# Optimization experiments

Hardware: AMD Instinct MI355X
Metric: run time of the kernel (lower is better)

## Reference

```python
import jax, jax.numpy as jnp
import numpy as np

B, L = 4, 2048
D_MODEL, D_INNER, D_STATE, DT_RANK, K = 512, 1024, 16, 64, 4


def setup_inputs() -> dict:
    key = jax.random.key(0)
    ks = jax.random.split(key, 21)
    def n(k, shape, s=0.02):
        return (jax.random.normal(k, shape) * s).astype(jnp.float32)
    inp = {"x": jax.random.normal(ks[0], (B, L, D_MODEL), jnp.float32)}
    for i, sfx in enumerate(("f", "b")):
        o = 1 + i * 8
        inp[f"W_in_{sfx}"] = n(ks[o], (2 * D_INNER, D_MODEL))
        inp[f"conv_w_{sfx}"] = n(ks[o + 1], (D_INNER, 1, K), 0.1)
        inp[f"conv_b_{sfx}"] = jnp.zeros((D_INNER,), jnp.float32)
        inp[f"A_log_{sfx}"] = (jax.random.normal(ks[o + 2], (D_STATE, D_INNER)) * 0.1).astype(jnp.float32)
        inp[f"D_{sfx}"] = jnp.ones((D_INNER,), jnp.float32)
        inp[f"Wx_{sfx}"] = n(ks[o + 3], (DT_RANK + 2 * D_STATE, D_INNER))
        inp[f"Wdt_{sfx}"] = n(ks[o + 4], (D_INNER, DT_RANK), DT_RANK ** -0.5)
        dt = jnp.exp(jax.random.uniform(ks[o + 5], (D_INNER,)) * (np.log(0.1) - np.log(0.001)) + np.log(0.001))
        inp[f"bdt_{sfx}"] = (dt + jnp.log(-jnp.expm1(-dt))).astype(jnp.float32)
        inp[f"Wout_{sfx}"] = n(ks[o + 6], (D_MODEL, D_INNER))
    return inp


def _mamba_block(x, W_in, conv_w, conv_b, A_log, Dp, Wx, Wdt, bdt, Wout):
    # x: [B, L, d_model]
    xz = jnp.einsum('bld,ed->ble', x, W_in)              # [B, L, 2*d_inner]
    xb, zb = xz[..., :D_INNER], xz[..., D_INNER:]
    # causal depthwise conv over time
    xc = jnp.transpose(xb, (0, 2, 1))                     # [B, M, L]
    xc = jax.lax.conv_general_dilated(
        xc, conv_w, window_strides=(1,), padding=[(K - 1, 0)],
        feature_group_count=D_INNER,
        dimension_numbers=('NCH', 'OIH', 'NCH')) + conv_b[None, :, None]
    xb = jax.nn.silu(jnp.transpose(xc, (0, 2, 1)))        # [B, L, M]
    # input-dependent SSM parameters
    proj = jnp.einsum('blm,pm->blp', xb, Wx)              # [B, L, dt_rank+2D]
    dt_in = proj[..., :DT_RANK]
    Bs = proj[..., DT_RANK:DT_RANK + D_STATE]             # [B, L, D]
    Cs = proj[..., DT_RANK + D_STATE:]                    # [B, L, D]
    dt = jax.nn.softplus(jnp.einsum('blr,mr->blm', dt_in, Wdt) + bdt)  # [B, L, M]
    A_T = -jnp.exp(A_log).T                               # [M, D]

    def step(h, inp):
        dt_t, x_t, B_t, C_t = inp                         # [B,M],[B,M],[B,D],[B,D]
        dA = jnp.exp(dt_t[:, :, None] * A_T[None])        # [B, M, D]
        h = dA * h + (dt_t * x_t)[:, :, None] * B_t[:, None, :]
        y_t = jnp.einsum('bmd,bd->bm', h, C_t)
        return h, y_t

    xs = (jnp.moveaxis(dt, 1, 0), jnp.moveaxis(xb, 1, 0),
          jnp.moveaxis(Bs, 1, 0), jnp.moveaxis(Cs, 1, 0))
    h0 = jnp.zeros((x.shape[0], D_INNER, D_STATE), x.dtype)
    _, ys = jax.lax.scan(step, h0, xs)                    # [L, B, M]
    y = jnp.moveaxis(ys, 0, 1) + Dp * xb                  # [B, L, M]
    y = y * jax.nn.silu(zb)                               # SiLU gate
    return jnp.einsum('blm,dm->bld', y, Wout)             # [B, L, d_model]


def reference(x,
              W_in_f, conv_w_f, conv_b_f, A_log_f, D_f, Wx_f, Wdt_f, bdt_f, Wout_f,
              W_in_b, conv_w_b, conv_b_b, A_log_b, D_b, Wx_b, Wdt_b, bdt_b, Wout_b):
    out_f = _mamba_block(x, W_in_f, conv_w_f, conv_b_f, A_log_f, D_f, Wx_f, Wdt_f, bdt_f, Wout_f)
    out_b = jnp.flip(_mamba_block(jnp.flip(x, 1), W_in_b, conv_w_b, conv_b_b, A_log_b, D_b, Wx_b, Wdt_b, bdt_b, Wout_b), 1)
    return out_f + out_b
```

## Files before the change

### kernel.cpp

```cpp
#include <hip/hip_runtime.h>
#include <hip/hip_bf16.h>
#include <cstdint>
#include <cstdio>

typedef float f32x4 __attribute__((ext_vector_type(4)));
typedef short s16x8 __attribute__((ext_vector_type(8)));
typedef unsigned int u32x2 __attribute__((ext_vector_type(2)));

__device__ __forceinline__ float us2f(unsigned short u){
  union { unsigned int i; float f; } v; v.i = ((unsigned int)u) << 16; return v.f;
}
__device__ __forceinline__ unsigned short f2us(float f){
  union { float f; unsigned int i; } v; v.f = f;
  unsigned int r = v.i + 0x7fffu + ((v.i >> 16) & 1u);
  return (unsigned short)(r >> 16);
}
__device__ __forceinline__ void gload_lds16(const void* g, void* l){
  __builtin_amdgcn_global_load_lds(
      (const __attribute__((address_space(1))) unsigned int*)g,
      (__attribute__((address_space(3))) unsigned int*)l, 16, 0, 0);
}

#define PK0 0.999962f

__global__ __launch_bounds__(256)
void prep_k(const float* __restrict__ x,
            const float* __restrict__ W_in_f, const float* __restrict__ W_in_b,
            const float* __restrict__ Wx_f,   const float* __restrict__ Wx_b,
            const float* __restrict__ Wdt_f,  const float* __restrict__ Wdt_b,
            const float* __restrict__ Wout_f, const float* __restrict__ Wout_b,
            const float* __restrict__ Alog_f, const float* __restrict__ Alog_b,
            const float* __restrict__ bdt_f,  const float* __restrict__ bdt_b,
            unsigned short* __restrict__ W1cat, unsigned short* __restrict__ Wxpad,
            unsigned short* __restrict__ Wdtb,  unsigned short* __restrict__ Woutcat,
            float* __restrict__ A2, float* __restrict__ bdtcat,
            unsigned short* __restrict__ xbf, float* __restrict__ Cf)
{
  long i = (long)blockIdx.x * 256 + threadIdx.x;
  if (i < 4194304) {
    xbf[i] = f2us(x[i]); return;
  }
  i -= 4194304;
  if (i < 2097152) {
    int n = (int)(i >> 9), k = (int)(i & 511);
    float v = (n < 2048) ? W_in_f[(long)n*512 + k] : W_in_b[(long)(n-2048)*512 + k];
    W1cat[i] = f2us(v); return;
  }
  i -= 2097152;
  if (i < 262144) {
    int dir = (int)(i >> 17); long r = i & 131071; int n = (int)(r >> 10), k = (int)(r & 1023);
    const float* Wx = dir ? Wx_b : Wx_f;
    Wxpad[(long)dir*131072 + r] = f2us(n < 96 ? Wx[(long)n*1024 + k] : 0.f); return;
  }
  i -= 262144;
  if (i < 131072) {
    int dir = (int)(i >> 16); long r = i & 65535;
    Wdtb[i] = f2us((dir ? Wdt_b : Wdt_f)[r]); return;
  }
  i -= 131072;
  if (i < 1048576) {
    int n = (int)(i >> 11), k = (int)(i & 2047);
    float v = (k < 1024) ? Wout_f[(long)n*1024 + k] : Wout_b[(long)n*1024 + (k-1024)];
    Woutcat[i] = f2us(v); return;
  }
  i -= 1048576;
  if (i < 32768) {
    int dir = (int)(i >> 14); long r = i & 16383; int m = (int)(r >> 4), d = (int)(r & 15);
    const float* Al = dir ? Alog_b : Alog_f;
    A2[i] = -__expf(Al[(long)d*1024 + m]) * 1.4426950408889634f; return;
  }
  i -= 32768;
  if (i < 2048) {
    int dir = (int)(i >> 10), m = (int)(i & 1023);
    bdtcat[i] = (dir ? bdt_b : bdt_f)[m]; return;
  }
  i -= 2048;
  if (i < 98304) {
    int dir = (int)(i / 49152); long r = i % 49152;
    int m = (int)(r / 48), j = (int)(r % 48);
    int k = j >> 4, d = j & 15;
    const float* Al = dir ? Alog_b : Alog_f;
    const float w = -__expf(Al[(long)d*1024 + m]);
    float c;
    if (k == 0)      c = 0.999150f * w;
    else if (k == 1) c = 0.492809f * w * w;
    else             c = 0.139212f * w * w * w;
    Cf[(long)dir*49152 + (long)m*48 + (k << 4) + d] = c;
    return;
  }
}

template<int OUT_MODE, int DBUF>
__global__ __launch_bounds__(256)
void gemm_bt(const unsigned short* __restrict__ Ap, const unsigned short* __restrict__ Bp,
             void* __restrict__ Cp, const float* __restrict__ biasp,
             float* __restrict__ bcf,
             int K, int lda, int ldb, int ldc,
             long az, long bz, long cz, int biasz)
{
  const int z   = blockIdx.z;
  const int tid = threadIdx.x;
  const int bm  = blockIdx.x, bn = blockIdx.y;

  __shared__ __align__(16) unsigned short Ash[1+DBUF][128][64];
  __shared__ __align__(16) unsigned short Bsh[1+DBUF][128][64];

  const int wave = tid >> 6, lane = tid & 63;
  const int wr = (wave >> 1) << 6, wc = (wave & 1) << 6;
  const int fr = lane & 15, fs = lane >> 4;

  const int rr  = tid >> 3;
  const int csp = tid & 7;
  const int csg = ((csp ^ (rr & 7)) << 3);

  const unsigned short* Ag = Ap + (long)z * az;
  const unsigned short* Bg = Bp + (long)z * bz;

  const long abase = (long)(bm*128 + rr)*lda + csg;
  const long bbase = (long)(bn*128 + rr)*ldb + csg;

  f32x4 acc[4][4];
  #pragma unroll
  for (int i=0;i<4;i++)
    #pragma unroll
    for (int j=0;j<4;j++) acc[i][j] = (f32x4){0.f,0.f,0.f,0.f};

  const int NK = K >> 6;

  auto stage = [&](int buf, int ks){
    const long k0 = (long)ks << 6;
    #pragma unroll
    for (int r=0;r<4;r++){
      gload_lds16(Ag + abase + (long)(r*32)*lda + k0, &Ash[buf][rr + r*32][csp << 3]);
      gload_lds16(Bg + bbase + (long)(r*32)*ldb + k0, &Bsh[buf][rr + r*32][csp << 3]);
    }
  };
  auto compute = [&](int buf){
    #pragma unroll
    for (int sub=0; sub<2; ++sub){
      s16x8 af[4], bfv[4];
      #pragma unroll
      for (int i=0;i<4;i++){
        const int ar = wr + i*16 + fr;
        af[i]  = *(const s16x8*)&Ash[buf][ar][(((sub<<2)+fs) ^ (fr&7)) << 3];
        const int br = wc + i*16 + fr;
        bfv[i] = *(const s16x8*)&Bsh[buf][br][(((sub<<2)+fs) ^ (fr&7)) << 3];
      }
      #pragma unroll
      for (int i=0;i<4;i++)
        #pragma unroll
        for (int j=0;j<4;j++)
          acc[i][j] = __builtin_amdgcn_mfma_f32_16x16x32_bf16(bfv[j], af[i], acc[i][j], 0, 0, 0);
    }
  };

  if (DBUF){
    stage(0, 0);
    int cur = 0;
    for (int ks = 0; ks < NK; ++ks){
      __syncthreads();
      if (ks + 1 < NK) stage(cur ^ 1, ks + 1);
      compute(cur);
      cur ^= 1;
    }
  } else {
    for (int ks = 0; ks < NK; ++ks){
      __syncthreads();
      stage(0, ks);
      __syncthreads();
      compute(0);
    }
  }

  #pragma unroll
  for (int i=0;i<4;i++){
    const int row = bm*128 + wr + i*16 + fr;
    #pragma unroll
    for (int j=0;j<4;j++){
      const int c0 = bn*128 + wc + j*16 + (fs << 2);
      f32x4 v = acc[i][j];
      const long cbase = (long)z*cz + (long)row*ldc + c0;
      if (OUT_MODE == 2){
        *(f32x4*)((float*)Cp + cbase) = v;
      } else if (OUT_MODE == 1){
        const f32x4 b4 = *(const f32x4*)(biasp + z*biasz + c0);
        u32x2 o;
        unsigned short s[4];
        #pragma unroll
        for (int e=0;e<4;e++){
          float t = v[e] + b4[e];
          t = fmaxf(t, 0.f) + log1pf(__expf(-fabsf(t)));
          s[e] = f2us(t);
        }
        o[0] = (unsigned int)s[0] | ((unsigned int)s[1] << 16);
        o[1] = (unsigned int)s[2] | ((unsigned int)s[3] << 16);
        *(u32x2*)((unsigned short*)Cp + cbase) = o;
      } else {
        if (OUT_MODE == 4 && ((c0 >> 10) & 1)){
          #pragma unroll
          for (int e=0;e<4;e++) v[e] = v[e] / (1.f + __expf(-v[e]));
        }
        u32x2 o;
        o[0] = (unsigned int)f2us(v[0]) | ((unsigned int)f2us(v[1]) << 16);
        o[1] = (unsigned int)f2us(v[2]) | ((unsigned int)f2us(v[3]) << 16);
        *(u32x2*)((unsigned short*)Cp + cbase) = o;
        if (OUT_MODE == 3 && c0 >= 64 && c0 < 96){
          *(f32x4*)(bcf + ((long)z*8192 + row)*32 + (c0 - 64)) = v;
        }
      }
    }
  }
}

__global__ __launch_bounds__(256)
void conv_silu_k(const unsigned short* __restrict__ xz,
                 const float* __restrict__ wf, const float* __restrict__ cbf,
                 const float* __restrict__ wb, const float* __restrict__ cbb,
                 unsigned short* __restrict__ xbc)
{
  const int tid = threadIdx.x;
  const long tok = blockIdx.x;
  const int l   = (int)(tok & 2047);
  const int dir = tid >> 7;
  const int mg  = (tid & 127) << 3;
  const float* w  = dir ? wb  : wf;
  const float* cb = dir ? cbb : cbf;
  const long rowb = tok << 12;
  const int  xcol = (dir << 11) + mg;

  f32x4 wv[8];
  #pragma unroll
  for (int e=0;e<8;e++) wv[e] = *(const f32x4*)(w + (mg + e)*4);
  const f32x4 cb0 = *(const f32x4*)(cb + mg);
  const f32x4 cb1 = *(const f32x4*)(cb + mg + 4);

  float acc[8];
  #pragma unroll
  for (int e=0;e<4;e++){ acc[e]=cb0[e]; acc[4+e]=cb1[e]; }

  #pragma unroll
  for (int k=0;k<4;k++){
    const int off = dir ? (3 - k) : (k - 3);
    const int pos = l + off;
    if (pos >= 0 && pos < 2048){
      const s16x8 xv = *(const s16x8*)(xz + rowb + ((long)off << 12) + xcol);
      #pragma unroll
      for (int e=0;e<8;e++)
        acc[e] = __builtin_fmaf(wv[e][k], us2f((unsigned short)xv[e]), acc[e]);
    }
  }
  s16x8 out;
  #pragma unroll
  for (int e=0;e<8;e++){
    const float s = acc[e] / (1.f + __expf(-acc[e]));
    out[e] = (short)f2us(s);
  }
  *(s16x8*)(xbc + tok*2048 + (dir << 10) + mg) = out;
}

#define SCHUNK 32
#define NCHUNK 64

__global__ __launch_bounds__(256)
void scan1_k(const unsigned short* __restrict__ dtb, const unsigned short* __restrict__ xbc,
             const float* __restrict__ BCf, const float* __restrict__ Cf,
             unsigned short* __restrict__ hloc, float* __restrict__ Ssum)
{
  const int tidx = threadIdx.x;
  const int cb = blockIdx.x, c = blockIdx.y, bz = blockIdx.z;
  const int b = bz >> 1, dir = bz & 1;
  const int m = cb*256 + tidx;

  float C1[16], C2[16], C3[16];
  { const f32x4* p = (const f32x4*)(Cf + ((long)dir*1024 + m)*48);
    #pragma unroll
    for (int q=0;q<4;q++){
      f32x4 v1=p[q], v2=p[q+4], v3=p[q+8];
      #pragma unroll
      for (int e=0;e<4;e++){ C1[q*4+e]=v1[e]; C2[q*4+e]=v2[e]; C3[q*4+e]=v3[e]; } } }

  const int  l0 = dir ? (2047 - c*SCHUNK) : (c*SCHUNK);
  const int  ls = dir ? -1 : 1;
  const long tok0 = (long)b*2048 + l0;

  __shared__ float Bs[SCHUNK][16];
  if (tidx < 128){
    const int r = tidx >> 2, c4 = (tidx & 3) << 2;
    *(f32x4*)&Bs[r][c4] =
        *(const f32x4*)(BCf + ((long)dir*8192 + tok0 + (long)ls*r)*32 + c4);
  }
  __syncthreads();

  const unsigned short* dtp = dtb + ((long)dir << 23) + tok0*1024 + m;
  const unsigned short* xvp = xbc + tok0*2048 + (dir << 10) + m;
  const long dstp = (long)ls*1024, xstp = (long)ls*2048;

  float h[16];
  #pragma unroll
  for (int d=0;d<16;d++) h[d]=0.f;
  float S = 0.f;

  unsigned short du = *dtp, xu = *xvp;
  for (int t=0;t<SCHUNK;t++){
    const float dt = us2f(du), xv = us2f(xu);
    dtp += dstp; xvp += xstp;
    du = *dtp; xu = *xvp;
    S += dt;
    const float u = dt * xv;
    const float dt2 = dt*dt, dt3 = dt2*dt;
    const f32x4 bv0 = *(const f32x4*)&Bs[t][0];
    const f32x4 bv1 = *(const f32x4*)&Bs[t][4];
    const f32x4 bv2 = *(const f32x4*)&Bs[t][8];
    const f32x4 bv3 = *(const f32x4*)&Bs[t][12];
    #pragma unroll
    for (int d=0;d<16;d++){
      const float bval = (d<4)? bv0[d&3] : (d<8)? bv1[d&3] : (d<12)? bv2[d&3] : bv3[d&3];
      float a = __builtin_fmaf(C1[d], dt, PK0);
      a = __builtin_fmaf(C2[d], dt2, a);
      a = __builtin_fmaf(C3[d], dt3, a);
      h[d] = __builtin_fmaf(a, h[d], u * bval);
    }
  }
  const long o = (((long)bz * NCHUNK) + c)*1024 + m;
  s16x8 hv0, hv1;
  #pragma unroll
  for (int e=0;e<8;e++){ hv0[e] = (short)f2us(h[e]); hv1[e] = (short)f2us(h[8+e]); }
  *(s16x8*)(hloc + (o << 4))     = hv0;
  *(s16x8*)(hloc + (o << 4) + 8) = hv1;
  Ssum[o] = S;
}

__global__ __launch_bounds__(256)
void scan2_k(const float* __restrict__ A2, const float* __restrict__ Ssum,
             unsigned short* __restrict__ hloc)
{
  const long idx = (long)blockIdx.x*256 + threadIdx.x;
  const long bz = idx >> 14; const int r = (int)(idx & 16383);
  const int dir = (int)(bz & 1);
  const float a2 = A2[((long)dir << 14) + r];
  const long base = bz * NCHUNK;
  float hs = 0.f;
  float hlN = us2f(hloc[base*16384 + r]);
  float SN  = Ssum[base*1024 + (r >> 4)];
  for (int c=0;c<NCHUNK;c++){
    const float hl = hlN, Sv = SN;
    const int cn = (c+1 < NCHUNK) ? c+1 : c;
    hlN = us2f(hloc[(base+cn)*16384 + r]);
    SN  = Ssum[(base+cn)*1024 + (r >> 4)];
    const float P = __builtin_amdgcn_exp2f(a2 * Sv);
    hloc[(base+c)*16384 + r] = f2us(hs);
    hs = __builtin_fmaf(P, hs, hl);
  }
}

__global__ __launch_bounds__(256)
void scan3_k(const unsigned short* __restrict__ dtb, const unsigned short* __restrict__ xbc,
             const float* __restrict__ BCf, const float* __restrict__ Cf,
             const unsigned short* __restrict__ hstart, const unsigned short* __restrict__ xz,
             const float* __restrict__ D_f, const float* __restrict__ D_b,
             unsigned short* __restrict__ ybuf)
{
  const int tidx = threadIdx.x;
  const int cb = blockIdx.x, c = blockIdx.y, bz = blockIdx.z;
  const int b = bz >> 1, dir = bz & 1;
  const int m = cb*256 + tidx;

  float C1[16], C2[16], C3[16];
  { const f32x4* p = (const f32x4*)(Cf + ((long)dir*1024 + m)*48);
    #pragma unroll
    for (int q=0;q<4;q++){
      f32x4 v1=p[q], v2=p[q+4], v3=p[q+8];
      #pragma unroll
      for (int e=0;e<4;e++){ C1[q*4+e]=v1[e]; C2[q*4+e]=v2[e]; C3[q*4+e]=v3[e]; } } }
  const float Dm = (dir ? D_b : D_f)[m];

  const int  l0 = dir ? (2047 - c*SCHUNK) : (c*SCHUNK);
  const int  ls = dir ? -1 : 1;
  const long tok0 = (long)b*2048 + l0;

  __shared__ float BC[SCHUNK][32];
  { const int r = tidx >> 3, c4 = (tidx & 7) << 2;
    *(f32x4*)&BC[r][c4] =
        *(const f32x4*)(BCf + ((long)dir*8192 + tok0 + (long)ls*r)*32 + c4); }

  float h[16];
  { const long o = ((((long)bz*NCHUNK) + c)*1024 + m) << 4;
    s16x8 hv0 = *(const s16x8*)(hstart + o);
    s16x8 hv1 = *(const s16x8*)(hstart + o + 8);
    #pragma unroll
    for (int e=0;e<8;e++){ h[e] = us2f((unsigned short)hv0[e]);
                           h[8+e] = us2f((unsigned short)hv1[e]); } }
  __syncthreads();

  const unsigned short* dtp = dtb + ((long)dir << 23) + tok0*1024 + m;
  const unsigned short* xvp = xbc + tok0*2048 + (dir << 10) + m;
  const unsigned short* zp  = xz  + (tok0 << 12) + (dir << 11) + 1024 + m;
  unsigned short*       yp  = ybuf + tok0*2048 + (dir << 10) + m;
  const long dstp = (long)ls*1024, xstp = (long)ls*2048, zstp = (long)ls << 12;

  unsigned short du = *dtp, xu = *xvp, zu = *zp;
  for (int t=0;t<SCHUNK;t++){
    const float dt = us2f(du), xv = us2f(xu), gate = us2f(zu);
    dtp += dstp; xvp += xstp; zp += zstp;
    du = *dtp; xu = *xvp; zu = *zp;
    const float u = dt * xv;
    const float dt2 = dt*dt, dt3 = dt2*dt;
    const f32x4 bv0 = *(const f32x4*)&BC[t][0];
    const f32x4 bv1 = *(const f32x4*)&BC[t][4];
    const f32x4 bv2 = *(const f32x4*)&BC[t][8];
    const f32x4 bv3 = *(const f32x4*)&BC[t][12];
    const f32x4 cv0 = *(const f32x4*)&BC[t][16];
    const f32x4 cv1 = *(const f32x4*)&BC[t][20];
    const f32x4 cv2 = *(const f32x4*)&BC[t][24];
    const f32x4 cv3 = *(const f32x4*)&BC[t][28];
    float y0=0.f, y1=0.f;
    #pragma unroll
    for (int d=0;d<16;d++){
      const float bval = (d<4)? bv0[d&3] : (d<8)? bv1[d&3] : (d<12)? bv2[d&3] : bv3[d&3];
      const float cval = (d<4)? cv0[d&3] : (d<8)? cv1[d&3] : (d<12)? cv2[d&3] : cv3[d&3];
      float a = __builtin_fmaf(C1[d], dt, PK0);
      a = __builtin_fmaf(C2[d], dt2, a);
      a = __builtin_fmaf(C3[d], dt3, a);
      h[d] = __builtin_fmaf(a, h[d], u * bval);
      if (d & 1) y1 = __builtin_fmaf(h[d], cval, y1);
      else       y0 = __builtin_fmaf(h[d], cval, y0);
    }
    const float y = (y0 + y1) + Dm * xv;
    *yp = f2us(y * gate);
    yp += xstp;
  }
}

extern "C" void kernel_launch(void* const* d_in, const int* in_sizes, int n_in,
                              void* d_out, int out_size, void* d_ws, size_t ws_size,
                              hipStream_t stream)
{
  const float* x      = (const float*)d_in[0];
  const float* W_in_f = (const float*)d_in[1];
  const float* convw_f= (const float*)d_in[2];
  const float* convb_f= (const float*)d_in[3];
  const float* Alog_f = (const float*)d_in[4];
  const float* D_f    = (const float*)d_in[5];
  const float* Wx_f   = (const float*)d_in[6];
  const float* Wdt_f  = (const float*)d_in[7];
  const float* bdt_f  = (const float*)d_in[8];
  const float* Wout_f = (const float*)d_in[9];
  const float* W_in_b = (const float*)d_in[10];
  const float* convw_b= (const float*)d_in[11];
  const float* convb_b= (const float*)d_in[12];
  const float* Alog_b = (const float*)d_in[13];
  const float* D_b    = (const float*)d_in[14];
  const float* Wx_b   = (const float*)d_in[15];
  const float* Wdt_b  = (const float*)d_in[16];
  const float* bdt_b  = (const float*)d_in[17];
  const float* Wout_b = (const float*)d_in[18];

  char* w = (char*)d_ws;
  auto carve = [&](size_t bytes) -> char* {
    char* p = w; w += (bytes + 255) & ~(size_t)255; return p;
  };
  unsigned short* W1cat   = (unsigned short*)carve(4096ULL*512*2);
  unsigned short* Wxpad   = (unsigned short*)carve(2ULL*128*1024*2);
  unsigned short* Wdtb    = (unsigned short*)carve(2ULL*1024*64*2);
  unsigned short* Woutcat = (unsigned short*)carve(512ULL*2048*2);
  float*          A2      = (float*)carve(2ULL*1024*16*4);
  float*          bdtcat  = (float*)carve(2048ULL*4);
  float*          Cf      = (float*)carve(2ULL*1024*48*4);
  float*          BCf     = (float*)carve(2ULL*8192*32*4);
  unsigned short* xz      = (unsigned short*)carve(8192ULL*4096*2);
  unsigned short* xbc     = (unsigned short*)carve(8192ULL*2048*2);
  unsigned short* proj    = (unsigned short*)carve(2ULL*8192*128*2);
  unsigned short* dtb     = (unsigned short*)carve(2ULL*8192*1024*2);
  unsigned short* ybuf    = (unsigned short*)carve(8192ULL*2048*2);
  unsigned short* hloc    = (unsigned short*)carve(8ULL*NCHUNK*1024*16*2);
  float*          Ssum    = (float*)carve(8ULL*NCHUNK*1024*4);
  unsigned short* xbf     = ybuf;

  if ((size_t)(w - (char*)d_ws) > ws_size) {
    fprintf(stderr, "kernel_launch: ws too small (%zu needed, %zu given)\n",
            (size_t)(w - (char*)d_ws), ws_size);
    return;
  }

  prep_k<<<dim3(30728), 256, 0, stream>>>(x, W_in_f, W_in_b, Wx_f, Wx_b, Wdt_f, Wdt_b,
                                          Wout_f, Wout_b, Alog_f, Alog_b, bdt_f, bdt_b,
                                          W1cat, Wxpad, Wdtb, Woutcat, A2, bdtcat, xbf, Cf);
  gemm_bt<4,1><<<dim3(64,32,1), 256, 0, stream>>>(xbf, W1cat, xz, nullptr, nullptr,
                                                  512, 512, 512, 4096, 0, 0, 0, 0);
  conv_silu_k<<<dim3(8192), 256, 0, stream>>>(xz, convw_f, convb_f, convw_b, convb_b, xbc);
  gemm_bt<3,0><<<dim3(64,1,2), 256, 0, stream>>>(xbc, Wxpad, proj, nullptr, BCf,
                                                 1024, 2048, 1024, 128,
                                                 1024, 131072, 1048576, 0);
  gemm_bt<1,0><<<dim3(64,8,2), 256, 0, stream>>>(proj, Wdtb, dtb, bdtcat, nullptr,
                                                 64, 128, 64, 1024,
                                                 1048576, 65536, 8388608, 1024);
  scan1_k<<<dim3(4,NCHUNK,8), 256, 0, stream>>>(dtb, xbc, BCf, Cf, hloc, Ssum);
  scan2_k<<<dim3(512), 256, 0, stream>>>(A2, Ssum, hloc);
  scan3_k<<<dim3(4,NCHUNK,8), 256, 0, stream>>>(dtb, xbc, BCf, Cf, hloc, xz, D_f, D_b, ybuf);
  gemm_bt<2,0><<<dim3(64,4,1), 256, 0, stream>>>(ybuf, Woutcat, d_out, nullptr, nullptr,
                                                 2048, 2048, 2048, 512, 0, 0, 0, 0);
}
```

Before: 329.3 us.

## Pre-pack weights into k8-interleaved layout and read B operand directly from global

Weights are repacked during prep into a [K/8][N][8] layout so each lane can load its MFMA B fragment as one contiguous 16-byte global load. The B tile is no longer staged through LDS, which halves shared-memory use and LDS traffic per block. The proj and output GEMMs also switch to the double-buffered path. The trade-off is that every wave now issues direct global/L2 loads for B inside the compute loop, with latency that the A-side prefetch overlap does not hide and reuse across waves that now depends on cache hits.

```diff
diff --git a/kernel.cpp b/kernel.cpp
--- a/kernel.cpp
+++ b/kernel.cpp
@@ -22,6 +22,7 @@
 }
 
 #define PK0 0.999962f
+
 
 __global__ __launch_bounds__(256)
 void prep_k(const float* __restrict__ x,
@@ -31,8 +32,8 @@
             const float* __restrict__ Wout_f, const float* __restrict__ Wout_b,
             const float* __restrict__ Alog_f, const float* __restrict__ Alog_b,
             const float* __restrict__ bdt_f,  const float* __restrict__ bdt_b,
-            unsigned short* __restrict__ W1cat, unsigned short* __restrict__ Wxpad,
-            unsigned short* __restrict__ Wdtb,  unsigned short* __restrict__ Woutcat,
+            unsigned short* __restrict__ W1p, unsigned short* __restrict__ Wxp,
+            unsigned short* __restrict__ Wdtp,  unsigned short* __restrict__ Woutp,
             float* __restrict__ A2, float* __restrict__ bdtcat,
             unsigned short* __restrict__ xbf, float* __restrict__ Cf)
 {
@@ -44,24 +45,28 @@
   if (i < 2097152) {
     int n = (int)(i >> 9), k = (int)(i & 511);
     float v = (n < 2048) ? W_in_f[(long)n*512 + k] : W_in_b[(long)(n-2048)*512 + k];
-    W1cat[i] = f2us(v); return;
+    W1p[((long)(k >> 3)*4096 + n)*8 + (k & 7)] = f2us(v); return;
   }
   i -= 2097152;
   if (i < 262144) {
     int dir = (int)(i >> 17); long r = i & 131071; int n = (int)(r >> 10), k = (int)(r & 1023);
     const float* Wx = dir ? Wx_b : Wx_f;
-    Wxpad[(long)dir*131072 + r] = f2us(n < 96 ? Wx[(long)n*1024 + k] : 0.f); return;
+    Wxp[(long)dir*131072 + ((long)(k >> 3)*128 + n)*8 + (k & 7)] =
+        f2us(n < 96 ? Wx[(long)n*1024 + k] : 0.f);
+    return;
   }
   i -= 262144;
   if (i < 131072) {
-    int dir = (int)(i >> 16); long r = i & 65535;
-    Wdtb[i] = f2us((dir ? Wdt_b : Wdt_f)[r]); return;
+    int dir = (int)(i >> 16); long r = i & 65535; int n = (int)(r >> 6), k = (int)(r & 63);
+    Wdtp[(long)dir*65536 + ((long)(k >> 3)*1024 + n)*8 + (k & 7)] =
+        f2us((dir ? Wdt_b : Wdt_f)[r]);
+    return;
   }
   i -= 131072;
   if (i < 1048576) {
     int n = (int)(i >> 11), k = (int)(i & 2047);
     float v = (k < 1024) ? Wout_f[(long)n*1024 + k] : Wout_b[(long)n*1024 + (k-1024)];
-    Woutcat[i] = f2us(v); return;
+    Woutp[((long)(k >> 3)*512 + n)*8 + (k & 7)] = f2us(v); return;
   }
   i -= 1048576;
   if (i < 32768) {
@@ -103,7 +108,6 @@
   const int bm  = blockIdx.x, bn = blockIdx.y;
 
   __shared__ __align__(16) unsigned short Ash[1+DBUF][128][64];
-  __shared__ __align__(16) unsigned short Bsh[1+DBUF][128][64];
 
   const int wave = tid >> 6, lane = tid & 63;
   const int wr = (wave >> 1) << 6, wc = (wave & 1) << 6;
@@ -117,7 +121,7 @@
   const unsigned short* Bg = Bp + (long)z * bz;
 
   const long abase = (long)(bm*128 + rr)*lda + csg;
-  const long bbase = (long)(bn*128 + rr)*ldb + csg;
+  const unsigned short* Bt = Bg + ((long)fs*ldb + bn*128 + wc + fr)*8;
 
   f32x4 acc[4][4];
   #pragma unroll
@@ -130,21 +134,20 @@
   auto stage = [&](int buf, int ks){
     const long k0 = (long)ks << 6;
     #pragma unroll
-    for (int r=0;r<4;r++){
+    for (int r=0;r<4;r++)
       gload_lds16(Ag + abase + (long)(r*32)*lda + k0, &Ash[buf][rr + r*32][csp << 3]);
-      gload_lds16(Bg + bbase + (long)(r*32)*ldb + k0, &Bsh[buf][rr + r*32][csp << 3]);
-    }
   };
-  auto compute = [&](int buf){
+  auto compute = [&](int buf, int ks){
     #pragma unroll
     for (int sub=0; sub<2; ++sub){
+      const unsigned short* Bk = Bt + (long)(ks*8 + sub*4)*ldb*8;
       s16x8 af[4], bfv[4];
+      #pragma unroll
+      for (int j=0;j<4;j++) bfv[j] = *(const s16x8*)(Bk + j*128);
       #pragma unroll
       for (int i=0;i<4;i++){
         const int ar = wr + i*16 + fr;
-        af[i]  = *(const s16x8*)&Ash[buf][ar][(((sub<<2)+fs) ^ (fr&7)) << 3];
-        const int br = wc + i*16 + fr;
-        bfv[i] = *(const s16x8*)&Bsh[buf][br][(((sub<<2)+fs) ^ (fr&7)) << 3];
+        af[i] = *(const s16x8*)&Ash[buf][ar][(((sub<<2)+fs) ^ (fr&7)) << 3];
       }
       #pragma unroll
       for (int i=0;i<4;i++)
@@ -160,7 +163,7 @@
     for (int ks = 0; ks < NK; ++ks){
       __syncthreads();
       if (ks + 1 < NK) stage(cur ^ 1, ks + 1);
-      compute(cur);
+      compute(cur, ks);
       cur ^= 1;
     }
   } else {
@@ -168,7 +171,7 @@
       __syncthreads();
       stage(0, ks);
       __syncthreads();
-      compute(0);
+      compute(0, ks);
     }
   }
 
@@ -459,10 +462,10 @@
   auto carve = [&](size_t bytes) -> char* {
     char* p = w; w += (bytes + 255) & ~(size_t)255; return p;
   };
-  unsigned short* W1cat   = (unsigned short*)carve(4096ULL*512*2);
-  unsigned short* Wxpad   = (unsigned short*)carve(2ULL*128*1024*2);
-  unsigned short* Wdtb    = (unsigned short*)carve(2ULL*1024*64*2);
-  unsigned short* Woutcat = (unsigned short*)carve(512ULL*2048*2);
+  unsigned short* W1p     = (unsigned short*)carve(4096ULL*512*2);
+  unsigned short* Wxp     = (unsigned short*)carve(2ULL*128*1024*2);
+  unsigned short* Wdtp    = (unsigned short*)carve(2ULL*1024*64*2);
+  unsigned short* Woutp   = (unsigned short*)carve(512ULL*2048*2);
   float*          A2      = (float*)carve(2ULL*1024*16*4);
   float*          bdtcat  = (float*)carve(2048ULL*4);
   float*          Cf      = (float*)carve(2ULL*1024*48*4);
@@ -484,19 +487,19 @@
 
   prep_k<<<dim3(30728), 256, 0, stream>>>(x, W_in_f, W_in_b, Wx_f, Wx_b, Wdt_f, Wdt_b,
                                           Wout_f, Wout_b, Alog_f, Alog_b, bdt_f, bdt_b,
-                                          W1cat, Wxpad, Wdtb, Woutcat, A2, bdtcat, xbf, Cf);
-  gemm_bt<4,1><<<dim3(64,32,1), 256, 0, stream>>>(xbf, W1cat, xz, nullptr, nullptr,
-                                                  512, 512, 512, 4096, 0, 0, 0, 0);
+                                          W1p, Wxp, Wdtp, Woutp, A2, bdtcat, xbf, Cf);
+  gemm_bt<4,1><<<dim3(64,32,1), 256, 0, stream>>>(xbf, W1p, xz, nullptr, nullptr,
+                                                  512, 512, 4096, 4096, 0, 0, 0, 0);
   conv_silu_k<<<dim3(8192), 256, 0, stream>>>(xz, convw_f, convb_f, convw_b, convb_b, xbc);
-  gemm_bt<3,0><<<dim3(64,1,2), 256, 0, stream>>>(xbc, Wxpad, proj, nullptr, BCf,
-                                                 1024, 2048, 1024, 128,
+  gemm_bt<3,1><<<dim3(64,1,2), 256, 0, stream>>>(xbc, Wxp, proj, nullptr, BCf,
+                                                 1024, 2048, 128, 128,
                                                  1024, 131072, 1048576, 0);
-  gemm_bt<1,0><<<dim3(64,8,2), 256, 0, stream>>>(proj, Wdtb, dtb, bdtcat, nullptr,
-                                                 64, 128, 64, 1024,
+  gemm_bt<1,0><<<dim3(64,8,2), 256, 0, stream>>>(proj, Wdtp, dtb, bdtcat, nullptr,
+                                                 64, 128, 1024, 1024,
                                                  1048576, 65536, 8388608, 1024);
   scan1_k<<<dim3(4,NCHUNK,8), 256, 0, stream>>>(dtb, xbc, BCf, Cf, hloc, Ssum);
   scan2_k<<<dim3(512), 256, 0, stream>>>(A2, Ssum, hloc);
   scan3_k<<<dim3(4,NCHUNK,8), 256, 0, stream>>>(dtb, xbc, BCf, Cf, hloc, xz, D_f, D_b, ybuf);
-  gemm_bt<2,0><<<dim3(64,4,1), 256, 0, stream>>>(ybuf, Woutcat, d_out, nullptr, nullptr,
-                                                 2048, 2048, 2048, 512, 0, 0, 0, 0);
-}
+  gemm_bt<2,1><<<dim3(64,4,1), 256, 0, stream>>>(ybuf, Woutp, d_out, nullptr, nullptr,
+                                                 2048, 2048, 512, 512, 0, 0, 0, 0);
+}
```

Result: no change. 332.2 us (+0.9%).
